# Kernel tuning notes

Hardware: AMD Instinct MI355X
Metric: run time of the kernel (lower is better)

The kernel has to match this reference:

```python
import jax, jax.numpy as jnp
import numpy as np

N_NODES = 8192
IN_DIM = 512
H_DIM = 128


def setup_inputs() -> dict:
    key = jax.random.key(0)
    k1, k2, k3, k4 = jax.random.split(key, 4)
    h = jax.random.normal(k1, (N_NODES, IN_DIM), dtype=jnp.float32)
    adj = jax.random.randint(k2, (N_NODES, N_NODES), 0, 2).astype(jnp.float32)
    # xavier-uniform-style scales
    w_scale = float(np.sqrt(6.0 / (IN_DIM + H_DIM)))
    W_w = jax.random.uniform(k3, (H_DIM, IN_DIM), minval=-w_scale, maxval=w_scale, dtype=jnp.float32)
    W_b = jnp.zeros((H_DIM,), dtype=jnp.float32)
    a_scale = float(np.sqrt(6.0 / (1 + H_DIM)))
    a = jax.random.uniform(k4, (1, H_DIM), minval=-a_scale, maxval=a_scale, dtype=jnp.float32)
    return {"h": h, "adj": adj, "W_w": W_w, "W_b": W_b, "a": a}


def reference(h, adj, W_w, W_b, a):
    # Wh: (n, H)
    Wh = h @ W_w.T + W_b
    # (Wh_i + Wh_j) @ a.T == s_i + s_j with s = Wh @ a.T  -> avoids (n,n,H) intermediate
    s = Wh @ a[0]                                  # (n,)
    e = jax.nn.leaky_relu(s[:, None] + s[None, :], negative_slope=0.2)  # (n, n)
    mask = adj != 0
    e = jnp.where(mask, e, -jnp.inf)
    # safe row softmax; rows with no neighbors -> alpha row of zeros (matches nan_to_num)
    m = jnp.max(e, axis=1, keepdims=True)
    m_safe = jnp.where(jnp.isfinite(m), m, 0.0)
    ex = jnp.where(mask, jnp.exp(e - m_safe), 0.0)
    denom = jnp.sum(ex, axis=1, keepdims=True)
    alpha = ex / jnp.where(denom == 0, 1.0, denom)
    z = jax.nn.sigmoid(alpha @ Wh)                 # (n, H)
    return z, alpha
```

## Files before the change

kernel.cpp:

```cpp
#include <hip/hip_runtime.h>
#include <hip/hip_bf16.h>
#include <math.h>

#define N_NODES 8192
#define IN_DIM  512
#define H_DIM   128
#define KC      1024
#define NKB     (N_NODES / KC)
#define BMRA    128
#define NTW     (N_NODES / 64)
#define NB_WH   (N_NODES / 32)
#define NB_MASK (N_NODES / 4)
#define NB_B    (N_NODES / 4)
#define NB_Z    ((N_NODES * H_DIM) / 256)

typedef __attribute__((ext_vector_type(8))) short bf16x8;
typedef __attribute__((ext_vector_type(4))) float f32x4;

__device__ __forceinline__ float lrelu(float x) { return fmaxf(x, 0.2f * x); }

__device__ __forceinline__ unsigned int f2mono(float x) {
    unsigned int b = __float_as_uint(x);
    return (b & 0x80000000u) ? ~b : (b | 0x80000000u);
}
__device__ __forceinline__ float mono2f(unsigned int u) {
    unsigned int b = (u & 0x80000000u) ? (u ^ 0x80000000u) : ~u;
    return __uint_as_float(b);
}

__device__ __forceinline__ short f2bf(float x) {
    union { __hip_bfloat16 h; short s; } cv;
    cv.h = __float2bfloat16(x);
    return cv.s;
}

__global__ __launch_bounds__(256) void k_front(const float* __restrict__ h,
                                               const float* __restrict__ Ww,
                                               const float* __restrict__ Wb,
                                               float* __restrict__ Wh,
                                               __hip_bfloat16* __restrict__ WhT2,
                                               const float* __restrict__ adj,
                                               unsigned long long* __restrict__ bm,
                                               f32x4* __restrict__ zp, int n16) {
    __shared__ float hT[64][32 + 4];
    __shared__ float wT[64][H_DIM + 4];
    const int tid = threadIdx.x;
    const int bx = blockIdx.x;

    if (bx < NB_WH) {
        const int w = tid >> 6, lane = tid & 63;
        const int trm = tid >> 5, tcm = tid & 31;
        const int row0 = bx * 32;

        float acc[4][4] = {};
        for (int k0 = 0; k0 < IN_DIM; k0 += 64) {
            __syncthreads();
            #pragma unroll
            for (int p = 0; p < 8; ++p) {
                int r = 4 * p + w;
                hT[lane][r] = h[(size_t)(row0 + r) * IN_DIM + k0 + lane];
            }
            #pragma unroll
            for (int p = 0; p < 32; ++p) {
                int c = 4 * p + w;
                wT[lane][c] = Ww[(size_t)c * IN_DIM + k0 + lane];
            }
            __syncthreads();
            #pragma unroll 8
            for (int kk = 0; kk < 64; ++kk) {
                f32x4 a4 = *(const f32x4*)&hT[kk][4 * trm];
                f32x4 b4 = *(const f32x4*)&wT[kk][4 * tcm];
                #pragma unroll
                for (int i = 0; i < 4; ++i)
                    #pragma unroll
                    for (int j = 0; j < 4; ++j)
                        acc[i][j] = fmaf(a4[i], b4[j], acc[i][j]);
            }
        }
        f32x4 wb4 = *(const f32x4*)&Wb[4 * tcm];
        #pragma unroll
        for (int i = 0; i < 4; ++i) {
            int row = row0 + 4 * trm + i;
            f32x4 v;
            #pragma unroll
            for (int jj = 0; jj < 4; ++jj) v[jj] = acc[i][jj] + wb4[jj];
            *(f32x4*)&Wh[(size_t)row * H_DIM + 4 * tcm] = v;
            int ts = row >> 5, kq = (row >> 3) & 3, e = row & 7;
            #pragma unroll
            for (int jj = 0; jj < 4; ++jj) {
                int c = 4 * tcm + jj;
                int f = c >> 4, r16 = c & 15;
                WhT2[((size_t)(ts * 8 + f) * 64 + kq * 16 + r16) * 8 + e] =
                    __float2bfloat16(v[jj]);
            }
        }
    } else if (bx < NB_WH + NB_MASK) {
        const int lane = tid & 63;
        const int row = (bx - NB_WH) * 4 + (tid >> 6);
        const float* arow = adj + (size_t)row * N_NODES;
        unsigned long long* mrow = bm + (size_t)row * NTW;
        #pragma unroll 4
        for (int c = 0; c < N_NODES / 256; ++c) {
            f32x4 a4 = __builtin_nontemporal_load((const f32x4*)(arow + c * 256 + lane * 4));
            unsigned long long v = 0ull;
            v |= (a4[0] != 0.f) ? 1ull : 0ull;
            v |= (a4[1] != 0.f) ? 2ull : 0ull;
            v |= (a4[2] != 0.f) ? 4ull : 0ull;
            v |= (a4[3] != 0.f) ? 8ull : 0ull;
            v <<= (4 * (lane & 15));
            v |= __shfl_xor(v, 1);
            v |= __shfl_xor(v, 2);
            v |= __shfl_xor(v, 4);
            v |= __shfl_xor(v, 8);
            if ((lane & 15) == 0)
                mrow[c * 4 + (lane >> 4)] = v;
        }
    } else {
        int i = (bx - NB_WH - NB_MASK) * 256 + tid;
        if (i < n16) {
            f32x4 zv = {0.f, 0.f, 0.f, 0.f};
            __builtin_nontemporal_store(zv, zp + i);
        }
    }
}

__global__ __launch_bounds__(256) void k_zero(f32x4* __restrict__ p, int n16) {
    int i = blockIdx.x * 256 + threadIdx.x;
    if (i < n16) {
        f32x4 zv = {0.f, 0.f, 0.f, 0.f};
        __builtin_nontemporal_store(zv, p + i);
    }
}

__global__ __launch_bounds__(256) void k_wh(const float* __restrict__ h,
                                            const float* __restrict__ Ww,
                                            const float* __restrict__ Wb,
                                            float* __restrict__ Wh,
                                            __hip_bfloat16* __restrict__ WhT2) {
    __shared__ float hT[64][32 + 4];
    __shared__ float wT[64][H_DIM + 4];
    const int tid = threadIdx.x;
    const int w = tid >> 6, lane = tid & 63;
    const int trm = tid >> 5, tcm = tid & 31;
    const int row0 = blockIdx.x * 32;

    float acc[4][4] = {};
    for (int k0 = 0; k0 < IN_DIM; k0 += 64) {
        __syncthreads();
        #pragma unroll
        for (int p = 0; p < 8; ++p) {
            int r = 4 * p + w;
            hT[lane][r] = h[(size_t)(row0 + r) * IN_DIM + k0 + lane];
        }
        #pragma unroll
        for (int p = 0; p < 32; ++p) {
            int c = 4 * p + w;
            wT[lane][c] = Ww[(size_t)c * IN_DIM + k0 + lane];
        }
        __syncthreads();
        #pragma unroll 8
        for (int kk = 0; kk < 64; ++kk) {
            f32x4 a4 = *(const f32x4*)&hT[kk][4 * trm];
            f32x4 b4 = *(const f32x4*)&wT[kk][4 * tcm];
            #pragma unroll
            for (int i = 0; i < 4; ++i)
                #pragma unroll
                for (int j = 0; j < 4; ++j)
                    acc[i][j] = fmaf(a4[i], b4[j], acc[i][j]);
        }
    }
    f32x4 wb4 = *(const f32x4*)&Wb[4 * tcm];
    #pragma unroll
    for (int i = 0; i < 4; ++i) {
        int row = row0 + 4 * trm + i;
        f32x4 v;
        #pragma unroll
        for (int jj = 0; jj < 4; ++jj) v[jj] = acc[i][jj] + wb4[jj];
        *(f32x4*)&Wh[(size_t)row * H_DIM + 4 * tcm] = v;
        int ts = row >> 5, kq = (row >> 3) & 3, e = row & 7;
        #pragma unroll
        for (int jj = 0; jj < 4; ++jj) {
            int c = 4 * tcm + jj;
            int f = c >> 4, r16 = c & 15;
            WhT2[((size_t)(ts * 8 + f) * 64 + kq * 16 + r16) * 8 + e] =
                __float2bfloat16(v[jj]);
        }
    }
}

__global__ __launch_bounds__(256) void k_s(const float* __restrict__ Wh,
                                           const float* __restrict__ a,
                                           float* __restrict__ s,
                                           unsigned int* __restrict__ smax) {
    const int w = threadIdx.x >> 6, lane = threadIdx.x & 63;
    const int row = blockIdx.x * 4 + w;
    float2 av = *(const float2*)&a[lane * 2];
    float2 wh = *(const float2*)&Wh[(size_t)row * H_DIM + lane * 2];
    float v = wh.x * av.x + wh.y * av.y;
    #pragma unroll
    for (int off = 32; off > 0; off >>= 1) v += __shfl_down(v, off);
    __shared__ float bmax[4];
    if (lane == 0) { s[row] = v; bmax[w] = v; }
    __syncthreads();
    if (threadIdx.x == 0) {
        float m = fmaxf(fmaxf(bmax[0], bmax[1]), fmaxf(bmax[2], bmax[3]));
        atomicMax(smax, f2mono(m));
    }
}

__global__ __launch_bounds__(256) void k_A(const unsigned long long* __restrict__ bm,
                                           const __hip_bfloat16* __restrict__ WhT2,
                                           const float* __restrict__ s,
                                           const unsigned int* __restrict__ smaxp,
                                           float* __restrict__ denom,
                                           float* __restrict__ y,
                                           float* __restrict__ ypart,
                                           int use_part) {
    const int lane = threadIdx.x & 63;
    const int w    = threadIdx.x >> 6;
    const int r16  = lane & 15;
    const int kq   = lane >> 4;
    const int rowB = blockIdx.x * BMRA + w * 32;
    const int j0   = blockIdx.y * KC;
    const int rowA0 = rowB + r16;
    const int rowA1 = rowB + 16 + r16;

    const float smax = mono2f(*smaxp);
    const float si0 = s[rowA0], si1 = s[rowA1];
    const float mi0 = lrelu(si0 + smax), mi1 = lrelu(si1 + smax);

    f32x4 acc0[8], acc1[8];
    {
        f32x4 zv = {0.f, 0.f, 0.f, 0.f};
        #pragma unroll
        for (int f = 0; f < 8; ++f) { acc0[f] = zv; acc1[f] = zv; }
    }
    float dsum0 = 0.f, dsum1 = 0.f;

    const float* sp = s + j0 + kq * 8;
    const unsigned long long* mrow0 = bm + (size_t)rowA0 * NTW + (j0 >> 6);
    const unsigned long long* mrow1 = bm + (size_t)rowA1 * NTW + (j0 >> 6);

    for (int bs = 0; bs < KC / 64; ++bs) {
        unsigned long long m64a = mrow0[bs];
        unsigned long long m64b = mrow1[bs];
        #pragma unroll
        for (int sub = 0; sub < 2; ++sub) {
            const int ts = bs * 2 + sub;
            unsigned int bits0 = (unsigned int)(m64a >> (sub * 32 + kq * 8)) & 0xffu;
            unsigned int bits1 = (unsigned int)(m64b >> (sub * 32 + kq * 8)) & 0xffu;

            f32x4 sc0 = *(const f32x4*)(sp + ts * 32);
            f32x4 sc1 = *(const f32x4*)(sp + ts * 32 + 4);
            float sv[8] = {sc0[0], sc0[1], sc0[2], sc0[3], sc1[0], sc1[1], sc1[2], sc1[3]};
            bf16x8 af0, af1;
            #pragma unroll
            for (int e = 0; e < 8; ++e) {
                float ex0 = ((bits0 >> e) & 1u) ? __expf(lrelu(si0 + sv[e]) - mi0) : 0.f;
                float ex1 = ((bits1 >> e) & 1u) ? __expf(lrelu(si1 + sv[e]) - mi1) : 0.f;
                dsum0 += ex0; dsum1 += ex1;
                af0[e] = f2bf(ex0);
                af1[e] = f2bf(ex1);
            }
            const __hip_bfloat16* base =
                WhT2 + (size_t)((j0 >> 5) + ts) * 4096 + lane * 8;
            #pragma unroll
            for (int half = 0; half < 2; ++half) {
                bf16x8 bc[4];
                #pragma unroll
                for (int f = 0; f < 4; ++f)
                    bc[f] = *(const bf16x8*)(base + (half * 4 + f) * 512);
                #pragma unroll
                for (int f = 0; f < 4; ++f) {
                    acc0[half * 4 + f] =
                        __builtin_amdgcn_mfma_f32_16x16x32_bf16(af0, bc[f], acc0[half * 4 + f], 0, 0, 0);
                    acc1[half * 4 + f] =
                        __builtin_amdgcn_mfma_f32_16x16x32_bf16(af1, bc[f], acc1[half * 4 + f], 0, 0, 0);
                }
            }
        }
    }

    {
        float v0 = dsum0, v1 = dsum1;
        v0 += __shfl_xor(v0, 16); v0 += __shfl_xor(v0, 32);
        v1 += __shfl_xor(v1, 16); v1 += __shfl_xor(v1, 32);
        if (lane < 16) {
            atomicAdd(&denom[rowB + lane], v0);
            atomicAdd(&denom[rowB + 16 + lane], v1);
        }
    }
    if (use_part) {
        float* yp = ypart + (size_t)blockIdx.y * N_NODES * H_DIM;
        #pragma unroll
        for (int f = 0; f < 8; ++f)
            #pragma unroll
            for (int i = 0; i < 4; ++i) {
                int cc = f * 16 + r16;
                yp[(size_t)(rowB + kq * 4 + i) * H_DIM + cc] = acc0[f][i];
                yp[(size_t)(rowB + 16 + kq * 4 + i) * H_DIM + cc] = acc1[f][i];
            }
    } else {
        #pragma unroll
        for (int f = 0; f < 8; ++f)
            #pragma unroll
            for (int i = 0; i < 4; ++i) {
                int cc = f * 16 + r16;
                atomicAdd(&y[(size_t)(rowB + kq * 4 + i) * H_DIM + cc], acc0[f][i]);
                atomicAdd(&y[(size_t)(rowB + 16 + kq * 4 + i) * H_DIM + cc], acc1[f][i]);
            }
    }
}

__global__ __launch_bounds__(256) void k_A_fb(const float* __restrict__ adj,
                                              const __hip_bfloat16* __restrict__ WhT2,
                                              const float* __restrict__ s,
                                              const unsigned int* __restrict__ smaxp,
                                              float* __restrict__ denom,
                                              float* __restrict__ y) {
    __shared__ unsigned char msk[64 * 64];
    const int tid  = threadIdx.x;
    const int lane = tid & 63;
    const int w    = tid >> 6;
    const int r16  = lane & 15;
    const int kq   = lane >> 4;
    const int row0 = blockIdx.x * 64;
    const int j0base = blockIdx.y * KC;
    const int rowA = row0 + w * 16 + r16;

    const float smax = mono2f(*smaxp);
    const float si = s[rowA];
    const float mi = lrelu(si + smax);

    f32x4 acc[8];
    {
        f32x4 zv = {0.f, 0.f, 0.f, 0.f};
        #pragma unroll
        for (int f = 0; f < 8; ++f) acc[f] = zv;
    }
    float dsum = 0.f;

    const float* sp = s + j0base + kq * 8;

    int sRow[4], sCol[4];
    #pragma unroll
    for (int p = 0; p < 4; ++p) {
        int seg = p * 256 + tid;
        sRow[p] = seg >> 4;
        sCol[p] = (seg & 15) * 4;
    }
    const int NBIG = KC / 64;
    f32x4 areg[4];
    #pragma unroll
    for (int p = 0; p < 4; ++p)
        areg[p] = __builtin_nontemporal_load(
            (const f32x4*)(adj + (size_t)(row0 + sRow[p]) * N_NODES + j0base + sCol[p]));

    for (int bs = 0; bs < NBIG; ++bs) {
        __syncthreads();
        #pragma unroll
        for (int p = 0; p < 4; ++p) {
            f32x4 a4 = areg[p];
            unsigned int mwd = 0u;
            mwd |= (a4[0] != 0.f) ? 0x00000001u : 0u;
            mwd |= (a4[1] != 0.f) ? 0x00000100u : 0u;
            mwd |= (a4[2] != 0.f) ? 0x00010000u : 0u;
            mwd |= (a4[3] != 0.f) ? 0x01000000u : 0u;
            int r = sRow[p], c = sCol[p];
            int slot = (c >> 3) ^ (r & 7);
            *(unsigned int*)&msk[r * 64 + (slot << 3) + (c & 7)] = mwd;
        }
        __syncthreads();
        if (bs + 1 < NBIG) {
            const int j1 = j0base + (bs + 1) * 64;
            #pragma unroll
            for (int p = 0; p < 4; ++p)
                areg[p] = __builtin_nontemporal_load(
                    (const f32x4*)(adj + (size_t)(row0 + sRow[p]) * N_NODES + j1 + sCol[p]));
        }
        #pragma unroll
        for (int sub = 0; sub < 2; ++sub) {
            const int ts = bs * 2 + sub;
            const int rT = w * 16 + r16;
            const int slotR = (sub * 4 + kq) ^ (r16 & 7);
            unsigned long long m8 = *(const unsigned long long*)&msk[rT * 64 + (slotR << 3)];
            unsigned int bits = (unsigned int)((m8 * 0x0102040810204080ull) >> 56) & 0xffu;

            f32x4 sc0 = *(const f32x4*)(sp + ts * 32);
            f32x4 sc1 = *(const f32x4*)(sp + ts * 32 + 4);
            float sv[8] = {sc0[0], sc0[1], sc0[2], sc0[3], sc1[0], sc1[1], sc1[2], sc1[3]};
            bf16x8 afrag;
            #pragma unroll
            for (int e = 0; e < 8; ++e) {
                bool nb = (bits >> e) & 1u;
                float ex = nb ? __expf(lrelu(si + sv[e]) - mi) : 0.f;
                dsum += ex;
                afrag[e] = f2bf(ex);
            }
            const __hip_bfloat16* base =
                WhT2 + (size_t)((j0base >> 5) + ts) * 4096 + lane * 8;
            #pragma unroll
            for (int half = 0; half < 2; ++half) {
                bf16x8 bc[4];
                #pragma unroll
                for (int f = 0; f < 4; ++f)
                    bc[f] = *(const bf16x8*)(base + (half * 4 + f) * 512);
                #pragma unroll
                for (int f = 0; f < 4; ++f)
                    acc[half * 4 + f] =
                        __builtin_amdgcn_mfma_f32_16x16x32_bf16(afrag, bc[f], acc[half * 4 + f], 0, 0, 0);
            }
        }
    }
    {
        float v = dsum;
        v += __shfl_xor(v, 16);
        v += __shfl_xor(v, 32);
        if (lane < 16) atomicAdd(&denom[row0 + w * 16 + lane], v);
    }
    #pragma unroll
    for (int f = 0; f < 8; ++f)
        #pragma unroll
        for (int i = 0; i < 4; ++i) {
            int rr = row0 + w * 16 + kq * 4 + i;
            int cc = f * 16 + r16;
            atomicAdd(&y[(size_t)rr * H_DIM + cc], acc[f][i]);
        }
}

__global__ __launch_bounds__(256) void k_back(const unsigned long long* __restrict__ bmask,
                                              const float* __restrict__ adj,
                                              const float* __restrict__ s,
                                              const float* __restrict__ denom,
                                              const unsigned int* __restrict__ smaxp,
                                              float* __restrict__ alpha,
                                              const float* __restrict__ ypart,
                                              const float* __restrict__ y,
                                              float* __restrict__ z,
                                              int use_mask, int use_part) {
    const int tid = threadIdx.x;
    const int bx = blockIdx.x;
    if (bx < NB_B) {
        const int NSTEP = N_NODES / 256;
        const int w = tid >> 6, lane = tid & 63;
        const int row = bx * 4 + w;
        const float smax = mono2f(*smaxp);
        const float si = s[row];
        const float mi = lrelu(si + smax);
        const float d = denom[row];
        const float rd = d > 0.f ? 1.f / d : 0.f;
        float* arow = alpha + (size_t)row * N_NODES;
        if (use_mask) {
            const unsigned long long* mrow = bmask + (size_t)row * NTW;
            #pragma unroll 4
            for (int t = 0; t < NSTEP; ++t) {
                int col = t * 256 + lane * 4;
                unsigned long long mb = mrow[t * 4 + (lane >> 4)];
                int sh = (lane & 15) * 4;
                f32x4 sj = *(const f32x4*)&s[col];
                f32x4 o;
                o[0] = ((mb >> (sh + 0)) & 1ull) ? __expf(lrelu(si + sj[0]) - mi) * rd : 0.f;
                o[1] = ((mb >> (sh + 1)) & 1ull) ? __expf(lrelu(si + sj[1]) - mi) * rd : 0.f;
                o[2] = ((mb >> (sh + 2)) & 1ull) ? __expf(lrelu(si + sj[2]) - mi) * rd : 0.f;
                o[3] = ((mb >> (sh + 3)) & 1ull) ? __expf(lrelu(si + sj[3]) - mi) * rd : 0.f;
                __builtin_nontemporal_store(o, (f32x4*)&arow[col]);
            }
        } else {
            const float* adjrow = adj + (size_t)row * N_NODES;
            #pragma unroll 4
            for (int t = 0; t < NSTEP; ++t) {
                int col = t * 256 + lane * 4;
                f32x4 a4 = __builtin_nontemporal_load((const f32x4*)&adjrow[col]);
                f32x4 sj = *(const f32x4*)&s[col];
                f32x4 o;
                o[0] = (a4[0] != 0.f) ? __expf(lrelu(si + sj[0]) - mi) * rd : 0.f;
                o[1] = (a4[1] != 0.f) ? __expf(lrelu(si + sj[1]) - mi) * rd : 0.f;
                o[2] = (a4[2] != 0.f) ? __expf(lrelu(si + sj[2]) - mi) * rd : 0.f;
                o[3] = (a4[3] != 0.f) ? __expf(lrelu(si + sj[3]) - mi) * rd : 0.f;
                __builtin_nontemporal_store(o, (f32x4*)&arow[col]);
            }
        }
    } else {
        int i = (bx - NB_B) * 256 + tid;
        int row = i >> 7;
        float d = denom[row];
        float rd = d > 0.f ? 1.f / d : 0.f;
        float v = 0.f;
        if (use_part) {
            #pragma unroll
            for (int p = 0; p < NKB; ++p)
                v += ypart[(size_t)p * N_NODES * H_DIM + i];
        } else {
            v = y[i];
        }
        v *= rd;
        z[i] = 1.f / (1.f + __expf(-v));
    }
}

extern "C" void kernel_launch(void* const* d_in, const int* in_sizes, int n_in,
                              void* d_out, int out_size, void* d_ws, size_t ws_size,
                              hipStream_t stream) {
    const float* h   = (const float*)d_in[0];
    const float* adj = (const float*)d_in[1];
    const float* Ww  = (const float*)d_in[2];
    const float* Wb  = (const float*)d_in[3];
    const float* a   = (const float*)d_in[4];

    float* z     = (float*)d_out;
    float* alpha = z + (size_t)N_NODES * H_DIM;

    char* ws = (char*)d_ws;
    float* y     = (float*)ws;  ws += sizeof(float) * (size_t)N_NODES * H_DIM;
    float* denom = (float*)ws;  ws += sizeof(float) * N_NODES;
    unsigned int* smax = (unsigned int*)ws;  ws += 256;
    size_t zero_bytes = (size_t)(ws - (char*)d_ws);
    float* Wh    = (float*)ws;  ws += sizeof(float) * (size_t)N_NODES * H_DIM;
    __hip_bfloat16* WhT2 = (__hip_bfloat16*)ws;
    ws += sizeof(__hip_bfloat16) * (size_t)N_NODES * H_DIM;
    float* s     = (float*)ws;  ws += sizeof(float) * N_NODES;
    unsigned long long* bmask = (unsigned long long*)ws;
    ws += (size_t)N_NODES * NTW * sizeof(unsigned long long);
    size_t mask_need = (size_t)(ws - (char*)d_ws);
    float* ypart = (float*)ws;
    ws += (size_t)NKB * N_NODES * H_DIM * sizeof(float);
    size_t part_need = (size_t)(ws - (char*)d_ws);
    int use_mask = (ws_size >= mask_need) ? 1 : 0;
    int use_part = (use_mask && ws_size >= part_need) ? 1 : 0;

    int n16 = (int)(zero_bytes / 16);
    int nbz = (n16 + 255) / 256;

    if (use_mask) {
        hipLaunchKernelGGL(k_front, dim3(NB_WH + NB_MASK + nbz), dim3(256), 0, stream,
                           h, Ww, Wb, Wh, WhT2, adj, bmask, (f32x4*)d_ws, n16);
        hipLaunchKernelGGL(k_s, dim3(N_NODES / 4), dim3(256), 0, stream, Wh, a, s, smax);
        hipLaunchKernelGGL(k_A, dim3(N_NODES / BMRA, NKB), dim3(256), 0, stream,
                           bmask, WhT2, s, smax, denom, y, ypart, use_part);
        hipLaunchKernelGGL(k_back, dim3(NB_B + NB_Z), dim3(256), 0, stream,
                           bmask, adj, s, denom, smax, alpha, ypart, y, z,
                           use_mask, use_part);
    } else {
        hipLaunchKernelGGL(k_zero, dim3(nbz), dim3(256), 0, stream, (f32x4*)d_ws, n16);
        hipLaunchKernelGGL(k_wh, dim3(NB_WH), dim3(256), 0, stream, h, Ww, Wb, Wh, WhT2);
        hipLaunchKernelGGL(k_s, dim3(N_NODES / 4), dim3(256), 0, stream, Wh, a, s, smax);
        hipLaunchKernelGGL(k_A_fb, dim3(N_NODES / 64, NKB), dim3(256), 0, stream,
                           adj, WhT2, s, smax, denom, y);
        hipLaunchKernelGGL(k_back, dim3(NB_B + NB_Z), dim3(256), 0, stream,
                           bmask, adj, s, denom, smax, alpha, ypart, y, z,
                           use_mask, use_part);
    }
}
```

Measured before the change: 234.7 us.

## Compute scores via folded W·a, fuse denom into mask pass, overlap alpha with MFMA

Scores s are now computed directly from h using a precomputed vector wa = Ww^T a plus a bias term. This removes the dependency on the full Wh product and the fp32 Wh write. With s ready before the front kernel, the softmax denominator is accumulated during the adjacency-to-bitmask pass, so the MFMA aggregation kernel no longer needs atomics or denom reductions. The alpha write blocks are co-scheduled in the same launch as the MFMA blocks, and the final z reduction gets its own kernel. This adds two small launches and recomputes exp in the mask pass in exchange for better overlap and fewer dependencies.

After: 231.7 us. Within noise of the previous version (-1.3%).

```diff
diff --git a/kernel.cpp b/kernel.cpp
--- a/kernel.cpp
+++ b/kernel.cpp
@@ -11,8 +11,8 @@
 #define NTW     (N_NODES / 64)
 #define NB_WH   (N_NODES / 32)
 #define NB_MASK (N_NODES / 4)
+#define NB_A    ((N_NODES / BMRA) * NKB)
 #define NB_B    (N_NODES / 4)
-#define NB_Z    ((N_NODES * H_DIM) / 256)
 
 typedef __attribute__((ext_vector_type(8))) short bf16x8;
 typedef __attribute__((ext_vector_type(4))) float f32x4;
@@ -34,14 +34,66 @@
     return cv.s;
 }
 
-__global__ __launch_bounds__(256) void k_front(const float* __restrict__ h,
-                                               const float* __restrict__ Ww,
-                                               const float* __restrict__ Wb,
-                                               float* __restrict__ Wh,
-                                               __hip_bfloat16* __restrict__ WhT2,
-                                               const float* __restrict__ adj,
-                                               unsigned long long* __restrict__ bm,
-                                               f32x4* __restrict__ zp, int n16) {
+__global__ __launch_bounds__(256) void k_wa(const float* __restrict__ Ww,
+                                            const float* __restrict__ Wb,
+                                            const float* __restrict__ a,
+                                            float* __restrict__ wa,
+                                            float* __restrict__ ba,
+                                            unsigned int* __restrict__ smax) {
+    const int t = threadIdx.x;
+    #pragma unroll
+    for (int kk = 0; kk < 2; ++kk) {
+        int k = t + kk * 256;
+        float sum = 0.f;
+        #pragma unroll 8
+        for (int c = 0; c < H_DIM; ++c)
+            sum += Ww[(size_t)c * IN_DIM + k] * a[c];
+        wa[k] = sum;
+    }
+    __shared__ float red[256];
+    red[t] = (t < H_DIM) ? Wb[t] * a[t] : 0.f;
+    __syncthreads();
+    for (int off = 128; off > 0; off >>= 1) {
+        if (t < off) red[t] += red[t + off];
+        __syncthreads();
+    }
+    if (t == 0) { ba[0] = red[0]; *smax = 0u; }
+}
+
+__global__ __launch_bounds__(256) void k_s0(const float* __restrict__ h,
+                                            const float* __restrict__ wa,
+                                            const float* __restrict__ ba,
+                                            float* __restrict__ s,
+                                            unsigned int* __restrict__ smax) {
+    const int w = threadIdx.x >> 6, lane = threadIdx.x & 63;
+    const int row = blockIdx.x * 4 + w;
+    const float* hp = h + (size_t)row * IN_DIM + lane * 8;
+    f32x4 h0 = *(const f32x4*)(hp);
+    f32x4 h1 = *(const f32x4*)(hp + 4);
+    f32x4 w0 = *(const f32x4*)(wa + lane * 8);
+    f32x4 w1 = *(const f32x4*)(wa + lane * 8 + 4);
+    float v = h0[0]*w0[0] + h0[1]*w0[1] + h0[2]*w0[2] + h0[3]*w0[3]
+            + h1[0]*w1[0] + h1[1]*w1[1] + h1[2]*w1[2] + h1[3]*w1[3];
+    #pragma unroll
+    for (int off = 32; off > 0; off >>= 1) v += __shfl_down(v, off);
+    __shared__ float bmax[4];
+    if (lane == 0) { float sv = v + ba[0]; s[row] = sv; bmax[w] = sv; }
+    __syncthreads();
+    if (threadIdx.x == 0) {
+        float m = fmaxf(fmaxf(bmax[0], bmax[1]), fmaxf(bmax[2], bmax[3]));
+        atomicMax(smax, f2mono(m));
+    }
+}
+
+__global__ __launch_bounds__(256) void k_front2(const float* __restrict__ h,
+                                                const float* __restrict__ Ww,
+                                                const float* __restrict__ Wb,
+                                                __hip_bfloat16* __restrict__ WhT2,
+                                                const float* __restrict__ adj,
+                                                unsigned long long* __restrict__ bm,
+                                                const float* __restrict__ s,
+                                                const unsigned int* __restrict__ smaxp,
+                                                float* __restrict__ denom) {
     __shared__ float hT[64][32 + 4];
     __shared__ float wT[64][H_DIM + 4];
     const int tid = threadIdx.x;
@@ -81,32 +133,36 @@
         #pragma unroll
         for (int i = 0; i < 4; ++i) {
             int row = row0 + 4 * trm + i;
-            f32x4 v;
-            #pragma unroll
-            for (int jj = 0; jj < 4; ++jj) v[jj] = acc[i][jj] + wb4[jj];
-            *(f32x4*)&Wh[(size_t)row * H_DIM + 4 * tcm] = v;
             int ts = row >> 5, kq = (row >> 3) & 3, e = row & 7;
             #pragma unroll
             for (int jj = 0; jj < 4; ++jj) {
                 int c = 4 * tcm + jj;
                 int f = c >> 4, r16 = c & 15;
                 WhT2[((size_t)(ts * 8 + f) * 64 + kq * 16 + r16) * 8 + e] =
-                    __float2bfloat16(v[jj]);
-            }
-        }
-    } else if (bx < NB_WH + NB_MASK) {
+                    __float2bfloat16(acc[i][jj] + wb4[jj]);
+            }
+        }
+    } else {
         const int lane = tid & 63;
         const int row = (bx - NB_WH) * 4 + (tid >> 6);
         const float* arow = adj + (size_t)row * N_NODES;
         unsigned long long* mrow = bm + (size_t)row * NTW;
+        const float smax = mono2f(*smaxp);
+        const float si = s[row];
+        const float mi = lrelu(si + smax);
+        float dsum = 0.f;
         #pragma unroll 4
         for (int c = 0; c < N_NODES / 256; ++c) {
-            f32x4 a4 = __builtin_nontemporal_load((const f32x4*)(arow + c * 256 + lane * 4));
+            int col = c * 256 + lane * 4;
+            f32x4 a4 = __builtin_nontemporal_load((const f32x4*)(arow + col));
+            f32x4 sj = *(const f32x4*)&s[col];
             unsigned long long v = 0ull;
-            v |= (a4[0] != 0.f) ? 1ull : 0ull;
-            v |= (a4[1] != 0.f) ? 2ull : 0ull;
-            v |= (a4[2] != 0.f) ? 4ull : 0ull;
-            v |= (a4[3] != 0.f) ? 8ull : 0ull;
+            #pragma unroll
+            for (int q = 0; q < 4; ++q) {
+                bool nb = (a4[q] != 0.f);
+                v |= nb ? (1ull << q) : 0ull;
+                dsum += nb ? __expf(lrelu(si + sj[q]) - mi) : 0.f;
+            }
             v <<= (4 * (lane & 15));
             v |= __shfl_xor(v, 1);
             v |= __shfl_xor(v, 2);
@@ -115,13 +171,134 @@
             if ((lane & 15) == 0)
                 mrow[c * 4 + (lane >> 4)] = v;
         }
+        #pragma unroll
+        for (int off = 32; off > 0; off >>= 1) dsum += __shfl_down(dsum, off);
+        if (lane == 0) denom[row] = dsum;
+    }
+}
+
+__global__ __launch_bounds__(256) void k_mid(const unsigned long long* __restrict__ bm,
+                                             const __hip_bfloat16* __restrict__ WhT2,
+                                             const float* __restrict__ s,
+                                             const unsigned int* __restrict__ smaxp,
+                                             const float* __restrict__ denom,
+                                             float* __restrict__ ypart,
+                                             float* __restrict__ alpha) {
+    const int tid = threadIdx.x;
+    const int bx = blockIdx.x;
+    const float smax = mono2f(*smaxp);
+
+    if (bx < NB_A) {
+        const int lane = tid & 63;
+        const int w    = tid >> 6;
+        const int r16  = lane & 15;
+        const int kq   = lane >> 4;
+        const int xb   = bx & 63;
+        const int yb   = bx >> 6;
+        const int rowB = xb * BMRA + w * 32;
+        const int j0   = yb * KC;
+        const int rowA0 = rowB + r16;
+        const int rowA1 = rowB + 16 + r16;
+
+        const float si0 = s[rowA0], si1 = s[rowA1];
+        const float mi0 = lrelu(si0 + smax), mi1 = lrelu(si1 + smax);
+
+        f32x4 acc0[8], acc1[8];
+        {
+            f32x4 zv = {0.f, 0.f, 0.f, 0.f};
+            #pragma unroll
+            for (int f = 0; f < 8; ++f) { acc0[f] = zv; acc1[f] = zv; }
+        }
+        const float* sp = s + j0 + kq * 8;
+        const unsigned long long* mrow0 = bm + (size_t)rowA0 * NTW + (j0 >> 6);
+        const unsigned long long* mrow1 = bm + (size_t)rowA1 * NTW + (j0 >> 6);
+
+        for (int bs = 0; bs < KC / 64; ++bs) {
+            unsigned long long m64a = mrow0[bs];
+            unsigned long long m64b = mrow1[bs];
+            #pragma unroll
+            for (int sub = 0; sub < 2; ++sub) {
+                const int ts = bs * 2 + sub;
+                unsigned int bits0 = (unsigned int)(m64a >> (sub * 32 + kq * 8)) & 0xffu;
+                unsigned int bits1 = (unsigned int)(m64b >> (sub * 32 + kq * 8)) & 0xffu;
+
+                f32x4 sc0 = *(const f32x4*)(sp + ts * 32);
+                f32x4 sc1 = *(const f32x4*)(sp + ts * 32 + 4);
+                float sv[8] = {sc0[0], sc0[1], sc0[2], sc0[3], sc1[0], sc1[1], sc1[2], sc1[3]};
+                bf16x8 af0, af1;
+                #pragma unroll
+                for (int e = 0; e < 8; ++e) {
+                    float ex0 = ((bits0 >> e) & 1u) ? __expf(lrelu(si0 + sv[e]) - mi0) : 0.f;
+                    float ex1 = ((bits1 >> e) & 1u) ? __expf(lrelu(si1 + sv[e]) - mi1) : 0.f;
+                    af0[e] = f2bf(ex0);
+                    af1[e] = f2bf(ex1);
+                }
+                const __hip_bfloat16* base =
+                    WhT2 + (size_t)((j0 >> 5) + ts) * 4096 + lane * 8;
+                #pragma unroll
+                for (int half = 0; half < 2; ++half) {
+                    bf16x8 bc[4];
+                    #pragma unroll
+                    for (int f = 0; f < 4; ++f)
+                        bc[f] = *(const bf16x8*)(base + (half * 4 + f) * 512);
+                    #pragma unroll
+                    for (int f = 0; f < 4; ++f) {
+                        acc0[half * 4 + f] =
+                            __builtin_amdgcn_mfma_f32_16x16x32_bf16(af0, bc[f], acc0[half * 4 + f], 0, 0, 0);
+                        acc1[half * 4 + f] =
+                            __builtin_amdgcn_mfma_f32_16x16x32_bf16(af1, bc[f], acc1[half * 4 + f], 0, 0, 0);
+                    }
+                }
+            }
+        }
+        float* yp = ypart + (size_t)yb * N_NODES * H_DIM;
+        #pragma unroll
+        for (int f = 0; f < 8; ++f)
+            #pragma unroll
+            for (int i = 0; i < 4; ++i) {
+                int cc = f * 16 + r16;
+                yp[(size_t)(rowB + kq * 4 + i) * H_DIM + cc] = acc0[f][i];
+                yp[(size_t)(rowB + 16 + kq * 4 + i) * H_DIM + cc] = acc1[f][i];
+            }
     } else {
-        int i = (bx - NB_WH - NB_MASK) * 256 + tid;
-        if (i < n16) {
-            f32x4 zv = {0.f, 0.f, 0.f, 0.f};
-            __builtin_nontemporal_store(zv, zp + i);
-        }
-    }
+        const int NSTEP = N_NODES / 256;
+        const int w = tid >> 6, lane = tid & 63;
+        const int row = (bx - NB_A) * 4 + w;
+        const float si = s[row];
+        const float mi = lrelu(si + smax);
+        const float d = denom[row];
+        const float rd = d > 0.f ? 1.f / d : 0.f;
+        float* arow = alpha + (size_t)row * N_NODES;
+        const unsigned long long* mrow = bm + (size_t)row * NTW;
+        #pragma unroll 4
+        for (int t = 0; t < NSTEP; ++t) {
+            int col = t * 256 + lane * 4;
+            unsigned long long mb = mrow[t * 4 + (lane >> 4)];
+            int sh = (lane & 15) * 4;
+            f32x4 sj = *(const f32x4*)&s[col];
+            f32x4 o;
+            o[0] = ((mb >> (sh + 0)) & 1ull) ? __expf(lrelu(si + sj[0]) - mi) * rd : 0.f;
+            o[1] = ((mb >> (sh + 1)) & 1ull) ? __expf(lrelu(si + sj[1]) - mi) * rd : 0.f;
+            o[2] = ((mb >> (sh + 2)) & 1ull) ? __expf(lrelu(si + sj[2]) - mi) * rd : 0.f;
+            o[3] = ((mb >> (sh + 3)) & 1ull) ? __expf(lrelu(si + sj[3]) - mi) * rd : 0.f;
+            __builtin_nontemporal_store(o, (f32x4*)&arow[col]);
+        }
+    }
+}
+
+__global__ __launch_bounds__(256) void k_z2(const float* __restrict__ ypart,
+                                            const float* __restrict__ denom,
+                                            float* __restrict__ z) {
+    int i = blockIdx.x * 256 + threadIdx.x;
+    int row = i >> 7;
+    float d = denom[row];
+    float rd = d > 0.f ? 1.f / d : 0.f;
+    float v = 0.f;
+    #pragma unroll
+    for (int p = 0; p < NKB; ++p)
+        v += ypart[(size_t)p * N_NODES * H_DIM + i];
+    v *= rd;
+    z[i] = 1.f / (1.f + __expf(-v));
 }
 
 __global__ __launch_bounds__(256) void k_zero(f32x4* __restrict__ p, int n16) {
@@ -132,11 +309,10 @@
     }
 }
 
-__global__ __launch_bounds__(256) void k_wh(const float* __restrict__ h,
-                                            const float* __restrict__ Ww,
-                                            const float* __restrict__ Wb,
-                                            float* __restrict__ Wh,
-                                            __hip_bfloat16* __restrict__ WhT2) {
+__global__ __launch_bounds__(256) void k_wh_fb(const float* __restrict__ h,
+                                               const float* __restrict__ Ww,
+                                               const float* __restrict__ Wb,
+                                               __hip_bfloat16* __restrict__ WhT2) {
     __shared__ float hT[64][32 + 4];
     __shared__ float wT[64][H_DIM + 4];
     const int tid = threadIdx.x;
@@ -173,142 +349,14 @@
     #pragma unroll
     for (int i = 0; i < 4; ++i) {
         int row = row0 + 4 * trm + i;
-        f32x4 v;
-        #pragma unroll
-        for (int jj = 0; jj < 4; ++jj) v[jj] = acc[i][jj] + wb4[jj];
-        *(f32x4*)&Wh[(size_t)row * H_DIM + 4 * tcm] = v;
         int ts = row >> 5, kq = (row >> 3) & 3, e = row & 7;
         #pragma unroll
         for (int jj = 0; jj < 4; ++jj) {
             int c = 4 * tcm + jj;
             int f = c >> 4, r16 = c & 15;
             WhT2[((size_t)(ts * 8 + f) * 64 + kq * 16 + r16) * 8 + e] =
-                __float2bfloat16(v[jj]);
-        }
-    }
-}
-
-__global__ __launch_bounds__(256) void k_s(const float* __restrict__ Wh,
-                                           const float* __restrict__ a,
-                                           float* __restrict__ s,
-                                           unsigned int* __restrict__ smax) {
-    const int w = threadIdx.x >> 6, lane = threadIdx.x & 63;
-    const int row = blockIdx.x * 4 + w;
-    float2 av = *(const float2*)&a[lane * 2];
-    float2 wh = *(const float2*)&Wh[(size_t)row * H_DIM + lane * 2];
-    float v = wh.x * av.x + wh.y * av.y;
-    #pragma unroll
-    for (int off = 32; off > 0; off >>= 1) v += __shfl_down(v, off);
-    __shared__ float bmax[4];
-    if (lane == 0) { s[row] = v; bmax[w] = v; }
-    __syncthreads();
-    if (threadIdx.x == 0) {
-        float m = fmaxf(fmaxf(bmax[0], bmax[1]), fmaxf(bmax[2], bmax[3]));
-        atomicMax(smax, f2mono(m));
-    }
-}
-
-__global__ __launch_bounds__(256) void k_A(const unsigned long long* __restrict__ bm,
-                                           const __hip_bfloat16* __restrict__ WhT2,
-                                           const float* __restrict__ s,
-                                           const unsigned int* __restrict__ smaxp,
-                                           float* __restrict__ denom,
-                                           float* __restrict__ y,
-                                           float* __restrict__ ypart,
-                                           int use_part) {
-    const int lane = threadIdx.x & 63;
-    const int w    = threadIdx.x >> 6;
-    const int r16  = lane & 15;
-    const int kq   = lane >> 4;
-    const int rowB = blockIdx.x * BMRA + w * 32;
-    const int j0   = blockIdx.y * KC;
-    const int rowA0 = rowB + r16;
-    const int rowA1 = rowB + 16 + r16;
-
-    const float smax = mono2f(*smaxp);
-    const float si0 = s[rowA0], si1 = s[rowA1];
-    const float mi0 = lrelu(si0 + smax), mi1 = lrelu(si1 + smax);
-
-    f32x4 acc0[8], acc1[8];
-    {
-        f32x4 zv = {0.f, 0.f, 0.f, 0.f};
-        #pragma unroll
-        for (int f = 0; f < 8; ++f) { acc0[f] = zv; acc1[f] = zv; }
-    }
-    float dsum0 = 0.f, dsum1 = 0.f;
-
-    const float* sp = s + j0 + kq * 8;
-    const unsigned long long* mrow0 = bm + (size_t)rowA0 * NTW + (j0 >> 6);
-    const unsigned long long* mrow1 = bm + (size_t)rowA1 * NTW + (j0 >> 6);
-
-    for (int bs = 0; bs < KC / 64; ++bs) {
-        unsigned long long m64a = mrow0[bs];
-        unsigned long long m64b = mrow1[bs];
-        #pragma unroll
-        for (int sub = 0; sub < 2; ++sub) {
-            const int ts = bs * 2 + sub;
-            unsigned int bits0 = (unsigned int)(m64a >> (sub * 32 + kq * 8)) & 0xffu;
-            unsigned int bits1 = (unsigned int)(m64b >> (sub * 32 + kq * 8)) & 0xffu;
-
-            f32x4 sc0 = *(const f32x4*)(sp + ts * 32);
-            f32x4 sc1 = *(const f32x4*)(sp + ts * 32 + 4);
-            float sv[8] = {sc0[0], sc0[1], sc0[2], sc0[3], sc1[0], sc1[1], sc1[2], sc1[3]};
-            bf16x8 af0, af1;
-            #pragma unroll
-            for (int e = 0; e < 8; ++e) {
-                float ex0 = ((bits0 >> e) & 1u) ? __expf(lrelu(si0 + sv[e]) - mi0) : 0.f;
-                float ex1 = ((bits1 >> e) & 1u) ? __expf(lrelu(si1 + sv[e]) - mi1) : 0.f;
-                dsum0 += ex0; dsum1 += ex1;
-                af0[e] = f2bf(ex0);
-                af1[e] = f2bf(ex1);
-            }
-            const __hip_bfloat16* base =
-                WhT2 + (size_t)((j0 >> 5) + ts) * 4096 + lane * 8;
-            #pragma unroll
-            for (int half = 0; half < 2; ++half) {
-                bf16x8 bc[4];
-                #pragma unroll
-                for (int f = 0; f < 4; ++f)
-                    bc[f] = *(const bf16x8*)(base + (half * 4 + f) * 512);
-                #pragma unroll
-                for (int f = 0; f < 4; ++f) {
-                    acc0[half * 4 + f] =
-                        __builtin_amdgcn_mfma_f32_16x16x32_bf16(af0, bc[f], acc0[half * 4 + f], 0, 0, 0);
-                    acc1[half * 4 + f] =
-                        __builtin_amdgcn_mfma_f32_16x16x32_bf16(af1, bc[f], acc1[half * 4 + f], 0, 0, 0);
-                }
-            }
-        }
-    }
-
-    {
-        float v0 = dsum0, v1 = dsum1;
-        v0 += __shfl_xor(v0, 16); v0 += __shfl_xor(v0, 32);
-        v1 += __shfl_xor(v1, 16); v1 += __shfl_xor(v1, 32);
-        if (lane < 16) {
-            atomicAdd(&denom[rowB + lane], v0);
-            atomicAdd(&denom[rowB + 16 + lane], v1);
-        }
-    }
-    if (use_part) {
-        float* yp = ypart + (size_t)blockIdx.y * N_NODES * H_DIM;
-        #pragma unroll
-        for (int f = 0; f < 8; ++f)
-            #pragma unroll
-            for (int i = 0; i < 4; ++i) {
-                int cc = f * 16 + r16;
-                yp[(size_t)(rowB + kq * 4 + i) * H_DIM + cc] = acc0[f][i];
-                yp[(size_t)(rowB + 16 + kq * 4 + i) * H_DIM + cc] = acc1[f][i];
-            }
-    } else {
-        #pragma unroll
-        for (int f = 0; f < 8; ++f)
-            #pragma unroll
-            for (int i = 0; i < 4; ++i) {
-                int cc = f * 16 + r16;
-                atomicAdd(&y[(size_t)(rowB + kq * 4 + i) * H_DIM + cc], acc0[f][i]);
-                atomicAdd(&y[(size_t)(rowB + 16 + kq * 4 + i) * H_DIM + cc], acc1[f][i]);
-            }
+                __float2bfloat16(acc[i][jj] + wb4[jj]);
+        }
     }
 }
 
@@ -339,7 +387,6 @@
         for (int f = 0; f < 8; ++f) acc[f] = zv;
     }
     float dsum = 0.f;
-
     const float* sp = s + j0base + kq * 8;
 
     int sRow[4], sCol[4];
@@ -428,74 +475,44 @@
         }
 }
 
-__global__ __launch_bounds__(256) void k_back(const unsigned long long* __restrict__ bmask,
-                                              const float* __restrict__ adj,
+__global__ __launch_bounds__(256) void k_B_fb(const float* __restrict__ adj,
                                               const float* __restrict__ s,
                                               const float* __restrict__ denom,
                                               const unsigned int* __restrict__ smaxp,
-                                              float* __restrict__ alpha,
-                                              const float* __restrict__ ypart,
-                                              const float* __restrict__ y,
-                                              float* __restrict__ z,
-                                              int use_mask, int use_part) {
-    const int tid = threadIdx.x;
-    const int bx = blockIdx.x;
-    if (bx < NB_B) {
-        const int NSTEP = N_NODES / 256;
-        const int w = tid >> 6, lane = tid & 63;
-        const int row = bx * 4 + w;
-        const float smax = mono2f(*smaxp);
-        const float si = s[row];
-        const float mi = lrelu(si + smax);
-        const float d = denom[row];
-        const float rd = d > 0.f ? 1.f / d : 0.f;
-        float* arow = alpha + (size_t)row * N_NODES;
-        if (use_mask) {
-            const unsigned long long* mrow = bmask + (size_t)row * NTW;
-            #pragma unroll 4
-            for (int t = 0; t < NSTEP; ++t) {
-                int col = t * 256 + lane * 4;
-                unsigned long long mb = mrow[t * 4 + (lane >> 4)];
-                int sh = (lane & 15) * 4;
-                f32x4 sj = *(const f32x4*)&s[col];
-                f32x4 o;
-                o[0] = ((mb >> (sh + 0)) & 1ull) ? __expf(lrelu(si + sj[0]) - mi) * rd : 0.f;
-                o[1] = ((mb >> (sh + 1)) & 1ull) ? __expf(lrelu(si + sj[1]) - mi) * rd : 0.f;
-                o[2] = ((mb >> (sh + 2)) & 1ull) ? __expf(lrelu(si + sj[2]) - mi) * rd : 0.f;
-                o[3] = ((mb >> (sh + 3)) & 1ull) ? __expf(lrelu(si + sj[3]) - mi) * rd : 0.f;
-                __builtin_nontemporal_store(o, (f32x4*)&arow[col]);
-            }
-        } else {
-            const float* adjrow = adj + (size_t)row * N_NODES;
-            #pragma unroll 4
-            for (int t = 0; t < NSTEP; ++t) {
-                int col = t * 256 + lane * 4;
-                f32x4 a4 = __builtin_nontemporal_load((const f32x4*)&adjrow[col]);
-                f32x4 sj = *(const f32x4*)&s[col];
-                f32x4 o;
-                o[0] = (a4[0] != 0.f) ? __expf(lrelu(si + sj[0]) - mi) * rd : 0.f;
-                o[1] = (a4[1] != 0.f) ? __expf(lrelu(si + sj[1]) - mi) * rd : 0.f;
-                o[2] = (a4[2] != 0.f) ? __expf(lrelu(si + sj[2]) - mi) * rd : 0.f;
-                o[3] = (a4[3] != 0.f) ? __expf(lrelu(si + sj[3]) - mi) * rd : 0.f;
-                __builtin_nontemporal_store(o, (f32x4*)&arow[col]);
-            }
-        }
-    } else {
-        int i = (bx - NB_B) * 256 + tid;
-        int row = i >> 7;
-        float d = denom[row];
-        float rd = d > 0.f ? 1.f / d : 0.f;
-        float v = 0.f;
-        if (use_part) {
-            #pragma unroll
-            for (int p = 0; p < NKB; ++p)
-                v += ypart[(size_t)p * N_NODES * H_DIM + i];
-        } else {
-            v = y[i];
-        }
-        v *= rd;
-        z[i] = 1.f / (1.f + __expf(-v));
-    }
+                                              float* __restrict__ alpha) {
+    const int NSTEP = N_NODES / 256;
+    const int w = threadIdx.x >> 6, lane = threadIdx.x & 63;
+    const int row = blockIdx.x * 4 + w;
+    const float smax = mono2f(*smaxp);
+    const float si = s[row];
+    const float mi = lrelu(si + smax);
+    const float d = denom[row];
+    const float rd = d > 0.f ? 1.f / d : 0.f;
+    float* arow = alpha + (size_t)row * N_NODES;
+    const float* adjrow = adj + (size_t)row * N_NODES;
+    #pragma unroll 4
+    for (int t = 0; t < NSTEP; ++t) {
+        int col = t * 256 + lane * 4;
+        f32x4 a4 = __builtin_nontemporal_load((const f32x4*)&adjrow[col]);
+        f32x4 sj = *(const f32x4*)&s[col];
+        f32x4 o;
+        o[0] = (a4[0] != 0.f) ? __expf(lrelu(si + sj[0]) - mi) * rd : 0.f;
+        o[1] = (a4[1] != 0.f) ? __expf(lrelu(si + sj[1]) - mi) * rd : 0.f;
+        o[2] = (a4[2] != 0.f) ? __expf(lrelu(si + sj[2]) - mi) * rd : 0.f;
+        o[3] = (a4[3] != 0.f) ? __expf(lrelu(si + sj[3]) - mi) * rd : 0.f;
+        __builtin_nontemporal_store(o, (f32x4*)&arow[col]);
+    }
+}
+
+__global__ __launch_bounds__(256) void k_z_fb(const float* __restrict__ y,
+                                              const float* __restrict__ denom,
+                                              float* __restrict__ z) {
+    int i = blockIdx.x * 256 + threadIdx.x;
+    int row = i >> 7;
+    float d = denom[row];
+    float rd = d > 0.f ? 1.f / d : 0.f;
+    float v = y[i] * rd;
+    z[i] = 1.f / (1.f + __expf(-v));
 }
 
 extern "C" void kernel_launch(void* const* d_in, const int* in_sizes, int n_in,
@@ -515,39 +532,38 @@
     float* denom = (float*)ws;  ws += sizeof(float) * N_NODES;
     unsigned int* smax = (unsigned int*)ws;  ws += 256;
     size_t zero_bytes = (size_t)(ws - (char*)d_ws);
-    float* Wh    = (float*)ws;  ws += sizeof(float) * (size_t)N_NODES * H_DIM;
+    float* wa    = (float*)ws;  ws += sizeof(float) * IN_DIM;
+    float* ba    = (float*)ws;  ws += 256;
     __hip_bfloat16* WhT2 = (__hip_bfloat16*)ws;
     ws += sizeof(__hip_bfloat16) * (size_t)N_NODES * H_DIM;
     float* s     = (float*)ws;  ws += sizeof(float) * N_NODES;
     unsigned long long* bmask = (unsigned long long*)ws;
     ws += (size_t)N_NODES * NTW * sizeof(unsigned long long);
-    size_t mask_need = (size_t)(ws - (char*)d_ws);
     float* ypart = (float*)ws;
     ws += (size_t)NKB * N_NODES * H_DIM * sizeof(float);
-    size_t part_need = (size_t)(ws - (char*)d_ws);
-    int use_mask = (ws_size >= mask_need) ? 1 : 0;
-    int use_part = (use_mask && ws_size >= part_need) ? 1 : 0;
-
-    int n16 = (int)(zero_bytes / 16);
-    int nbz = (n16 + 255) / 256;
-
-    if (use_mask) {
-        hipLaunchKernelGGL(k_front, dim3(NB_WH + NB_MASK + nbz), dim3(256), 0, stream,
-                           h, Ww, Wb, Wh, WhT2, adj, bmask, (f32x4*)d_ws, n16);
-        hipLaunchKernelGGL(k_s, dim3(N_NODES / 4), dim3(256), 0, stream, Wh, a, s, smax);
-        hipLaunchKernelGGL(k_A, dim3(N_NODES / BMRA, NKB), dim3(256), 0, stream,
-                           bmask, WhT2, s, smax, denom, y, ypart, use_part);
-        hipLaunchKernelGGL(k_back, dim3(NB_B + NB_Z), dim3(256), 0, stream,
-                           bmask, adj, s, denom, smax, alpha, ypart, y, z,
-                           use_mask, use_part);
+    size_t full_need = (size_t)(ws - (char*)d_ws);
+    int use_full = (ws_size >= full_need) ? 1 : 0;
+
+    hipLaunchKernelGGL(k_wa, dim3(1), dim3(256), 0, stream, Ww, Wb, a, wa, ba, smax);
+    hipLaunchKernelGGL(k_s0, dim3(N_NODES / 4), dim3(256), 0, stream, h, wa, ba, s, smax);
+
+    if (use_full) {
+        hipLaunchKernelGGL(k_front2, dim3(NB_WH + NB_MASK), dim3(256), 0, stream,
+                           h, Ww, Wb, WhT2, adj, bmask, s, smax, denom);
+        hipLaunchKernelGGL(k_mid, dim3(NB_A + NB_B), dim3(256), 0, stream,
+                           bmask, WhT2, s, smax, denom, ypart, alpha);
+        hipLaunchKernelGGL(k_z2, dim3((N_NODES * H_DIM) / 256), dim3(256), 0, stream,
+                           ypart, denom, z);
     } else {
-        hipLaunchKernelGGL(k_zero, dim3(nbz), dim3(256), 0, stream, (f32x4*)d_ws, n16);
-        hipLaunchKernelGGL(k_wh, dim3(NB_WH), dim3(256), 0, stream, h, Ww, Wb, Wh, WhT2);
-        hipLaunchKernelGGL(k_s, dim3(N_NODES / 4), dim3(256), 0, stream, Wh, a, s, smax);
+        int n16 = (int)(zero_bytes / 16);
+        hipLaunchKernelGGL(k_zero, dim3((n16 + 255) / 256), dim3(256), 0, stream,
+                           (f32x4*)d_ws, n16);
+        hipLaunchKernelGGL(k_wh_fb, dim3(NB_WH), dim3(256), 0, stream, h, Ww, Wb, WhT2);
         hipLaunchKernelGGL(k_A_fb, dim3(N_NODES / 64, NKB), dim3(256), 0, stream,
                            adj, WhT2, s, smax, denom, y);
-        hipLaunchKernelGGL(k_back, dim3(NB_B + NB_Z), dim3(256), 0, stream,
-                           bmask, adj, s, denom, smax, alpha, ypart, y, z,
-                           use_mask, use_part);
-    }
-}
+        hipLaunchKernelGGL(k_B_fb, dim3(N_NODES / 4), dim3(256), 0, stream,
+                           adj, s, denom, smax, alpha);
+        hipLaunchKernelGGL(k_z_fb, dim3((N_NODES * H_DIM) / 256), dim3(256), 0, stream,
+                           y, denom, z);
+    }
+}
```
